# Kernel tuning notes

Measured on AMD Instinct MI355X. Metric: run time of the kernel, lower is better.

## Reference

```python
import jax, jax.numpy as jnp
import numpy as np

D_MODEL = 1024
NUM_HEADS = 16
HEAD_DIM = D_MODEL // NUM_HEADS


def setup_inputs() -> dict:
    key = jax.random.key(0)
    ks = jax.random.split(key, 5)
    x = jax.random.normal(ks[0], (2, 2048, D_MODEL), dtype=jnp.float32)
    # torch nn.Linear init scale ~ U(-1/sqrt(in), 1/sqrt(in)); use small normals
    s = 1.0 / np.sqrt(D_MODEL)
    W_qkv = jax.random.normal(ks[1], (D_MODEL, 3 * D_MODEL), dtype=jnp.float32) * s
    b_qkv = jax.random.normal(ks[2], (3 * D_MODEL,), dtype=jnp.float32) * s
    W_out = jax.random.normal(ks[3], (D_MODEL, D_MODEL), dtype=jnp.float32) * s
    b_out = jax.random.normal(ks[4], (D_MODEL,), dtype=jnp.float32) * s
    return {"x": x, "W_qkv": W_qkv, "b_qkv": b_qkv, "W_out": W_out, "b_out": b_out}


def reference(x, W_qkv, b_qkv, W_out, b_out):
    B, S, _ = x.shape
    qkv = x @ W_qkv + b_qkv                                  # [B,S,3D]
    qkv = qkv.reshape(B, S, NUM_HEADS, 3 * HEAD_DIM).transpose(0, 2, 1, 3)  # [B,H,S,3d]
    q, k, v = jnp.split(qkv, 3, axis=-1)                     # each [B,H,S,d]
    scale = 1.0 / np.sqrt(HEAD_DIM)
    scores = jnp.einsum("bhqd,bhkd->bhqk", q, k) * scale      # [B,H,S,S]
    attn = jax.nn.softmax(scores, axis=-1)
    values = jnp.einsum("bhqk,bhkd->bhqd", attn, v)           # [B,H,S,d]
    values = values.transpose(0, 2, 1, 3).reshape(B, S, D_MODEL)
    return values @ W_out + b_out
```

## Files before the change

### kernel.cpp

```cpp
#include <hip/hip_runtime.h>


#define D_MODEL 1024
#define NHEAD   16
#define HDIM    64
#define SEQ     2048
#define BATCH   2
#define NTOK    (BATCH * SEQ)

typedef float    f32x4 __attribute__((ext_vector_type(4)));
typedef _Float16 f16x8 __attribute__((ext_vector_type(8)));
typedef _Float16 f16x4 __attribute__((ext_vector_type(4)));

#define GLOBAL_LOAD_LDS16(gptr, lptr)                                            \
    __builtin_amdgcn_global_load_lds(                                            \
        (const __attribute__((address_space(1))) unsigned int*)(gptr),           \
        (__attribute__((address_space(3))) unsigned int*)(lptr), 16, 0, 0)

__global__ __launch_bounds__(256) void prep_kernel(
    const float* __restrict__ x, _Float16* __restrict__ xh,
    const float* __restrict__ Wqkv, _Float16* __restrict__ wq_t,
    const float* __restrict__ Wout, _Float16* __restrict__ wo_t)
{
    const int bx = blockIdx.x;
    const int tid = threadIdx.x;
    if (bx < 4096) {
        const int i = (bx * 256 + tid) * 4;
        const float4 v = *(const float4*)&x[i];
        f16x4 hh;
        hh[0] = (_Float16)v.x; hh[1] = (_Float16)v.y;
        hh[2] = (_Float16)v.z; hh[3] = (_Float16)v.w;
        *(f16x4*)&xh[i] = hh;
        return;
    }
    __shared__ float ts[64][65];
    const float* W; _Float16* Wt; int N, n0, k0;
    if (bx < 4096 + 768) {
        const int local = bx - 4096;
        W = Wqkv; Wt = wq_t; N = 3072;
        n0 = (local % 48) * 64; k0 = (local / 48) * 64;
    } else {
        const int local = bx - 4864;
        W = Wout; Wt = wo_t; N = 1024;
        n0 = (local % 16) * 64; k0 = (local / 16) * 64;
    }
    {
        const int r = tid >> 2, c = (tid & 3) << 4;
        const float* src = W + (size_t)(k0 + r) * N + n0 + c;
        #pragma unroll
        for (int u = 0; u < 4; ++u)
            *(float4*)&ts[r][c + u * 4] = *(const float4*)&src[u * 4];
    }
    __syncthreads();
    {
        const int n = tid >> 2, kg = (tid & 3) << 4;
        f16x8 v0, v1;
        #pragma unroll
        for (int j = 0; j < 8; ++j) {
            v0[j] = (_Float16)ts[kg + j][n];
            v1[j] = (_Float16)ts[kg + 8 + j][n];
        }
        _Float16* dst = Wt + (size_t)(n0 + n) * D_MODEL + k0 + kg;
        *(f16x8*)&dst[0] = v0;
        *(f16x8*)&dst[8] = v1;
    }
}

__global__ __launch_bounds__(512) void gemm_qkv_kernel(
    const _Float16* __restrict__ A, const _Float16* __restrict__ Bt,
    const float* __restrict__ bias, _Float16* __restrict__ Cout,
    int M, int N, int K)
{
    __shared__ _Float16 lds[2][4096];
    const int tid = threadIdx.x;
    const int wave = tid >> 6, lane = tid & 63;
    const int quad = lane >> 4, l16 = lane & 15;
    const int m0 = blockIdx.y * 128, n0 = blockIdx.x * 128;
    const int wr = wave >> 1, wc = wave & 1;

    f32x4 acc[2][4] = {};

    const bool isA = wave < 4;
    const _Float16* gsrc = isA ? (A + (size_t)m0 * K) : (Bt + (size_t)n0 * K);
    _Float16* ldst = isA ? &lds[0][0] : &lds[1][0];
    const int sbase = (wave & 3) * 2;

    for (int k0 = 0; k0 < K; k0 += 32) {
        __syncthreads();
        #pragma unroll
        for (int j = 0; j < 2; ++j) {
            const int seg = sbase + j;
            const int chunk = seg >> 1;
            const int row = ((seg & 1) << 6) | lane;
            GLOBAL_LOAD_LDS16(gsrc + (size_t)row * K + k0 + chunk * 8, ldst + seg * 512);
        }
        __syncthreads();

        f16x8 a[2], b[4];
        #pragma unroll
        for (int mt = 0; mt < 2; ++mt)
            a[mt] = *(const f16x8*)&lds[0][quad * 1024 + (wr * 32 + mt * 16 + l16) * 8];
        #pragma unroll
        for (int nt = 0; nt < 4; ++nt)
            b[nt] = *(const f16x8*)&lds[1][quad * 1024 + (wc * 64 + nt * 16 + l16) * 8];
        #pragma unroll
        for (int mt = 0; mt < 2; ++mt)
            #pragma unroll
            for (int nt = 0; nt < 4; ++nt)
                acc[mt][nt] = __builtin_amdgcn_mfma_f32_16x16x32_f16(a[mt], b[nt], acc[mt][nt], 0, 0, 0);
    }

    #pragma unroll
    for (int nt = 0; nt < 4; ++nt) {
        const int col = n0 + wc * 64 + nt * 16 + l16;
        const float bv = bias[col];
        #pragma unroll
        for (int mt = 0; mt < 2; ++mt) {
            #pragma unroll
            for (int r = 0; r < 4; ++r) {
                const int row = m0 + wr * 32 + mt * 16 + quad * 4 + r;
                Cout[(size_t)row * N + col] = (_Float16)(acc[mt][nt][r] + bv);
            }
        }
    }
}

__global__ __launch_bounds__(512) void gemm_out_kernel(
    const _Float16* __restrict__ A, const _Float16* __restrict__ Bt,
    const float* __restrict__ bias, float* __restrict__ Cout)
{
    const int K = D_MODEL, N = D_MODEL;
    __shared__ _Float16 ldsA[4096];
    __shared__ _Float16 ldsB[2048];
    const int tid = threadIdx.x;
    const int wave = tid >> 6, lane = tid & 63;
    const int quad = lane >> 4, l16 = lane & 15;
    const int m0 = blockIdx.y * 128, n0 = blockIdx.x * 64;
    const int wr = wave >> 1, wc = wave & 1;

    f32x4 acc[2][2] = {};

    for (int k0 = 0; k0 < K; k0 += 32) {
        __syncthreads();
        if (wave < 4) {
            #pragma unroll
            for (int j = 0; j < 2; ++j) {
                const int seg = wave * 2 + j;
                const int chunk = seg >> 1;
                const int row = ((seg & 1) << 6) | lane;
                GLOBAL_LOAD_LDS16(A + (size_t)(m0 + row) * K + k0 + chunk * 8, ldsA + seg * 512);
            }
        } else {
            const int seg = wave - 4;
            GLOBAL_LOAD_LDS16(Bt + (size_t)(n0 + lane) * K + k0 + seg * 8, ldsB + seg * 512);
        }
        __syncthreads();

        f16x8 a[2], b[2];
        #pragma unroll
        for (int mt = 0; mt < 2; ++mt)
            a[mt] = *(const f16x8*)&ldsA[quad * 1024 + (wr * 32 + mt * 16 + l16) * 8];
        #pragma unroll
        for (int nt = 0; nt < 2; ++nt)
            b[nt] = *(const f16x8*)&ldsB[quad * 512 + (wc * 32 + nt * 16 + l16) * 8];
        #pragma unroll
        for (int mt = 0; mt < 2; ++mt)
            #pragma unroll
            for (int nt = 0; nt < 2; ++nt)
                acc[mt][nt] = __builtin_amdgcn_mfma_f32_16x16x32_f16(a[mt], b[nt], acc[mt][nt], 0, 0, 0);
    }

    #pragma unroll
    for (int nt = 0; nt < 2; ++nt) {
        const int col = n0 + wc * 32 + nt * 16 + l16;
        const float bv = bias[col];
        #pragma unroll
        for (int mt = 0; mt < 2; ++mt) {
            #pragma unroll
            for (int r = 0; r < 4; ++r) {
                const int row = m0 + wr * 32 + mt * 16 + quad * 4 + r;
                Cout[(size_t)row * N + col] = acc[mt][nt][r] + bv;
            }
        }
    }
}

__global__ __launch_bounds__(256) void swizzle_kv_kernel(
    const _Float16* __restrict__ qkv,
    _Float16* __restrict__ Ksw, _Float16* __restrict__ Vsw)
{
    __shared__ _Float16 ts[64][72];
    const int tid = threadIdx.x;
    const int s0 = blockIdx.x * 64, h = blockIdx.y, b = blockIdx.z;
    const size_t hsz = (size_t)8 * SEQ * 8;
    _Float16* kh = Ksw + (size_t)(b * NHEAD + h) * hsz;
    _Float16* vh = Vsw + (size_t)(b * NHEAD + h) * hsz;

    {
        const int s = s0 + (tid >> 2);
        const int dg = (tid & 3) << 4;
        const _Float16* src = qkv + (size_t)(b * SEQ + s) * (3 * D_MODEL) + h * (3 * HDIM) + HDIM + dg;
        const f16x8 v0 = *(const f16x8*)&src[0];
        const f16x8 v1 = *(const f16x8*)&src[8];
        const int c0 = dg >> 3;
        *(f16x8*)&kh[((size_t)c0 * SEQ + s) * 8]       = v0;
        *(f16x8*)&kh[((size_t)(c0 + 1) * SEQ + s) * 8] = v1;
    }
    {
        const int s = tid >> 2, dg = (tid & 3) << 4;
        const _Float16* src = qkv + (size_t)(b * SEQ + s0 + s) * (3 * D_MODEL) + h * (3 * HDIM) + 2 * HDIM + dg;
        *(f16x8*)&ts[s][dg]     = *(const f16x8*)&src[0];
        *(f16x8*)&ts[s][dg + 8] = *(const f16x8*)&src[8];
    }
    __syncthreads();
    {
        const int d = tid >> 2, sg = (tid & 3) << 4;
        f16x8 v0, v1;
        #pragma unroll
        for (int j = 0; j < 8; ++j) { v0[j] = ts[sg + j][d]; v1[j] = ts[sg + 8 + j][d]; }
        const int cs0 = (s0 + sg) >> 3;
        *(f16x8*)&vh[((size_t)cs0 * HDIM + d) * 8]       = v0;
        *(f16x8*)&vh[((size_t)(cs0 + 1) * HDIM + d) * 8] = v1;
    }
}

__global__ __launch_bounds__(256) void attn_mfma_kernel(
    const _Float16* __restrict__ qkv,
    const _Float16* __restrict__ Ksw, const _Float16* __restrict__ Vsw,
    _Float16* __restrict__ val)
{
    __shared__ _Float16 Ks[8 * 64 * 8];
    __shared__ _Float16 Vts[8 * 64 * 8];
    __shared__ _Float16 Ps[64 * 72];

    const int tid = threadIdx.x;
    const int wave = tid >> 6, lane = tid & 63;
    const int quad = lane >> 4, l16 = lane & 15;
    const int qt = blockIdx.x, h = blockIdx.y, b = blockIdx.z;
    const int q0 = qt * 64;

    const size_t hsz = (size_t)8 * SEQ * 8;
    const _Float16* kh = Ksw + (size_t)(b * NHEAD + h) * hsz;
    const _Float16* vh = Vsw + (size_t)(b * NHEAD + h) * hsz;

    f16x8 qf[2];
    {
        const int row = q0 + wave * 16 + l16;
        const _Float16* src = qkv + (size_t)(b * SEQ + row) * (3 * D_MODEL) + h * (3 * HDIM) + quad * 8;
        const f16x8 t0 = *(const f16x8*)(src);
        const f16x8 t1 = *(const f16x8*)(src + 32);
        #pragma unroll
        for (int j = 0; j < 8; ++j) {
            qf[0][j] = (_Float16)((float)t0[j] * 0.1803368802f);
            qf[1][j] = (_Float16)((float)t1[j] * 0.1803368802f);
        }
    }

    f32x4 acc[4] = {};
    float rs = 0.f;

    for (int kt = 0; kt < SEQ / 64; ++kt) {
        __syncthreads();
        #pragma unroll
        for (int jj = 0; jj < 2; ++jj) {
            const int c = wave * 2 + jj;
            GLOBAL_LOAD_LDS16(kh + ((size_t)c * SEQ + kt * 64 + lane) * 8, Ks + c * 512);
            GLOBAL_LOAD_LDS16(vh + ((size_t)(kt * 8 + c) * HDIM + lane) * 8, Vts + c * 512);
        }
        __syncthreads();

        f32x4 s[4] = {};
        #pragma unroll
        for (int mt = 0; mt < 4; ++mt) {
            const f16x8 kA0 = *(const f16x8*)&Ks[quad * 512 + (mt * 16 + l16) * 8];
            const f16x8 kA1 = *(const f16x8*)&Ks[(4 + quad) * 512 + (mt * 16 + l16) * 8];
            s[mt] = __builtin_amdgcn_mfma_f32_16x16x32_f16(kA0, qf[0], s[mt], 0, 0, 0);
            s[mt] = __builtin_amdgcn_mfma_f32_16x16x32_f16(kA1, qf[1], s[mt], 0, 0, 0);
        }

        #pragma unroll
        for (int mt = 0; mt < 4; ++mt) {
            const float p0 = __builtin_amdgcn_exp2f(s[mt][0]);
            const float p1 = __builtin_amdgcn_exp2f(s[mt][1]);
            const float p2 = __builtin_amdgcn_exp2f(s[mt][2]);
            const float p3 = __builtin_amdgcn_exp2f(s[mt][3]);
            rs += (p0 + p1) + (p2 + p3);
            uint2 w;
            w.x = __builtin_bit_cast(unsigned, __builtin_amdgcn_cvt_pkrtz(p0, p1));
            w.y = __builtin_bit_cast(unsigned, __builtin_amdgcn_cvt_pkrtz(p2, p3));
            *(uint2*)&Ps[(wave * 16 + l16) * 72 + mt * 16 + quad * 4] = w;
        }

        const f16x8 pA0 = *(const f16x8*)&Ps[(wave * 16 + l16) * 72 + quad * 8];
        const f16x8 pA1 = *(const f16x8*)&Ps[(wave * 16 + l16) * 72 + 32 + quad * 8];
        #pragma unroll
        for (int nt = 0; nt < 4; ++nt) {
            const f16x8 v0 = *(const f16x8*)&Vts[quad * 512 + (nt * 16 + l16) * 8];
            const f16x8 v1 = *(const f16x8*)&Vts[(4 + quad) * 512 + (nt * 16 + l16) * 8];
            acc[nt] = __builtin_amdgcn_mfma_f32_16x16x32_f16(pA0, v0, acc[nt], 0, 0, 0);
            acc[nt] = __builtin_amdgcn_mfma_f32_16x16x32_f16(pA1, v1, acc[nt], 0, 0, 0);
        }
    }

    rs += __shfl_xor(rs, 16);
    rs += __shfl_xor(rs, 32);
    const float inv = 1.f / rs;
    float invr[4];
    #pragma unroll
    for (int r = 0; r < 4; ++r)
        invr[r] = __shfl(inv, quad * 4 + r, 16);

    #pragma unroll
    for (int r = 0; r < 4; ++r) {
        const int row = b * SEQ + q0 + wave * 16 + quad * 4 + r;
        #pragma unroll
        for (int nt = 0; nt < 4; ++nt) {
            const int col = h * HDIM + nt * 16 + l16;
            val[(size_t)row * D_MODEL + col] = (_Float16)(acc[nt][r] * invr[r]);
        }
    }
}

extern "C" void kernel_launch(void* const* d_in, const int* in_sizes, int n_in,
                              void* d_out, int out_size, void* d_ws, size_t ws_size,
                              hipStream_t stream)
{
    const float* x     = (const float*)d_in[0];
    const float* W_qkv = (const float*)d_in[1];
    const float* b_qkv = (const float*)d_in[2];
    const float* W_out = (const float*)d_in[3];
    const float* b_out = (const float*)d_in[4];

    char* ws = (char*)d_ws;
    _Float16* Ksw   = (_Float16*)ws;
    _Float16* val_h = (_Float16*)(ws + (8u << 20));
    _Float16* wq_t  = (_Float16*)(ws + (16u << 20));
    _Float16* wo_t  = (_Float16*)(ws + (22u << 20));
    _Float16* qkv_h = (_Float16*)(ws + (24u << 20));
    _Float16* x_h   = (_Float16*)(ws + (48u << 20));
    _Float16* Vsw   = (_Float16*)(ws + (48u << 20));

    prep_kernel<<<5120, 256, 0, stream>>>(x, x_h, W_qkv, wq_t, W_out, wo_t);
    gemm_qkv_kernel<<<dim3(3 * D_MODEL / 128, NTOK / 128), 512, 0, stream>>>(
        x_h, wq_t, b_qkv, qkv_h, NTOK, 3 * D_MODEL, D_MODEL);
    swizzle_kv_kernel<<<dim3(SEQ / 64, NHEAD, BATCH), 256, 0, stream>>>(qkv_h, Ksw, Vsw);
    attn_mfma_kernel<<<dim3(SEQ / 64, NHEAD, BATCH), 256, 0, stream>>>(qkv_h, Ksw, Vsw, val_h);
    gemm_out_kernel<<<dim3(D_MODEL / 64, NTOK / 128), 512, 0, stream>>>(
        val_h, wo_t, b_out, (float*)d_out);
}
```

Measured before the change: 226.2 us.

## Use 32x32 MFMA, 128-row query tiles, and double-buffered K/V in attention

The attention kernel moves from 16x16x32 to 32x32x16 MFMA instructions, with each wave now owning 32 query rows and each block 128. The grid is halved, so each K/V tile loaded into LDS is reused across twice as many queries. K/V loads into LDS are double-buffered, with the next tile prefetched while the current one is computed, leaving one barrier per iteration instead of two. The softmax still has no max subtraction, as before. The trade-off is fewer blocks (512) for occupancy, more accumulator registers, and more LDS per block.

```diff
diff --git a/kernel.cpp b/kernel.cpp
--- a/kernel.cpp
+++ b/kernel.cpp
@@ -8,9 +8,10 @@
 #define BATCH   2
 #define NTOK    (BATCH * SEQ)
 
-typedef float    f32x4 __attribute__((ext_vector_type(4)));
-typedef _Float16 f16x8 __attribute__((ext_vector_type(8)));
-typedef _Float16 f16x4 __attribute__((ext_vector_type(4)));
+typedef float    f32x4  __attribute__((ext_vector_type(4)));
+typedef float    f32x16 __attribute__((ext_vector_type(16)));
+typedef _Float16 f16x8  __attribute__((ext_vector_type(8)));
+typedef _Float16 f16x4  __attribute__((ext_vector_type(4)));
 
 #define GLOBAL_LOAD_LDS16(gptr, lptr)                                            \
     __builtin_amdgcn_global_load_lds(                                            \
@@ -229,95 +230,118 @@
     const _Float16* __restrict__ Ksw, const _Float16* __restrict__ Vsw,
     _Float16* __restrict__ val)
 {
-    __shared__ _Float16 Ks[8 * 64 * 8];
-    __shared__ _Float16 Vts[8 * 64 * 8];
-    __shared__ _Float16 Ps[64 * 72];
+    __shared__ _Float16 Ks[2][4096];
+    __shared__ _Float16 Vts[2][4096];
+    __shared__ _Float16 Ps[128 * 72];
 
     const int tid = threadIdx.x;
     const int wave = tid >> 6, lane = tid & 63;
-    const int quad = lane >> 4, l16 = lane & 15;
+    const int l31 = lane & 31, hi = lane >> 5;
     const int qt = blockIdx.x, h = blockIdx.y, b = blockIdx.z;
-    const int q0 = qt * 64;
+    const int q0 = qt * 128;
 
     const size_t hsz = (size_t)8 * SEQ * 8;
     const _Float16* kh = Ksw + (size_t)(b * NHEAD + h) * hsz;
     const _Float16* vh = Vsw + (size_t)(b * NHEAD + h) * hsz;
 
-    f16x8 qf[2];
-    {
-        const int row = q0 + wave * 16 + l16;
-        const _Float16* src = qkv + (size_t)(b * SEQ + row) * (3 * D_MODEL) + h * (3 * HDIM) + quad * 8;
-        const f16x8 t0 = *(const f16x8*)(src);
-        const f16x8 t1 = *(const f16x8*)(src + 32);
-        #pragma unroll
-        for (int j = 0; j < 8; ++j) {
-            qf[0][j] = (_Float16)((float)t0[j] * 0.1803368802f);
-            qf[1][j] = (_Float16)((float)t1[j] * 0.1803368802f);
-        }
-    }
-
-    f32x4 acc[4] = {};
+    f16x8 qf[4];
+    {
+        const int row = q0 + wave * 32 + l31;
+        const _Float16* src = qkv + (size_t)(b * SEQ + row) * (3 * D_MODEL) + h * (3 * HDIM) + hi * 8;
+        #pragma unroll
+        for (int kk = 0; kk < 4; ++kk) {
+            const f16x8 t = *(const f16x8*)(src + kk * 16);
+            #pragma unroll
+            for (int j = 0; j < 8; ++j)
+                qf[kk][j] = (_Float16)((float)t[j] * 0.1803368802f);
+        }
+    }
+
+    f32x16 acc0 = {};
+    f32x16 acc1 = {};
     float rs = 0.f;
 
+    _Float16* const psrow = &Ps[(wave * 32 + l31) * 72];
+
+    #pragma unroll
+    for (int jj = 0; jj < 2; ++jj) {
+        const int c = wave * 2 + jj;
+        GLOBAL_LOAD_LDS16(kh + ((size_t)c * SEQ + lane) * 8, &Ks[0][c * 512]);
+        GLOBAL_LOAD_LDS16(vh + ((size_t)c * HDIM + lane) * 8, &Vts[0][c * 512]);
+    }
+    __syncthreads();
+
     for (int kt = 0; kt < SEQ / 64; ++kt) {
-        __syncthreads();
-        #pragma unroll
-        for (int jj = 0; jj < 2; ++jj) {
-            const int c = wave * 2 + jj;
-            GLOBAL_LOAD_LDS16(kh + ((size_t)c * SEQ + kt * 64 + lane) * 8, Ks + c * 512);
-            GLOBAL_LOAD_LDS16(vh + ((size_t)(kt * 8 + c) * HDIM + lane) * 8, Vts + c * 512);
-        }
-        __syncthreads();
-
-        f32x4 s[4] = {};
-        #pragma unroll
-        for (int mt = 0; mt < 4; ++mt) {
-            const f16x8 kA0 = *(const f16x8*)&Ks[quad * 512 + (mt * 16 + l16) * 8];
-            const f16x8 kA1 = *(const f16x8*)&Ks[(4 + quad) * 512 + (mt * 16 + l16) * 8];
-            s[mt] = __builtin_amdgcn_mfma_f32_16x16x32_f16(kA0, qf[0], s[mt], 0, 0, 0);
-            s[mt] = __builtin_amdgcn_mfma_f32_16x16x32_f16(kA1, qf[1], s[mt], 0, 0, 0);
-        }
-
-        #pragma unroll
-        for (int mt = 0; mt < 4; ++mt) {
-            const float p0 = __builtin_amdgcn_exp2f(s[mt][0]);
-            const float p1 = __builtin_amdgcn_exp2f(s[mt][1]);
-            const float p2 = __builtin_amdgcn_exp2f(s[mt][2]);
-            const float p3 = __builtin_amdgcn_exp2f(s[mt][3]);
+        const int cur = kt & 1;
+
+        if (kt + 1 < SEQ / 64) {
+            #pragma unroll
+            for (int jj = 0; jj < 2; ++jj) {
+                const int c = wave * 2 + jj;
+                GLOBAL_LOAD_LDS16(kh + ((size_t)c * SEQ + (kt + 1) * 64 + lane) * 8,
+                                  &Ks[cur ^ 1][c * 512]);
+                GLOBAL_LOAD_LDS16(vh + ((size_t)((kt + 1) * 8 + c) * HDIM + lane) * 8,
+                                  &Vts[cur ^ 1][c * 512]);
+            }
+        }
+
+        f32x16 s0 = {};
+        f32x16 s1 = {};
+        #pragma unroll
+        for (int kk = 0; kk < 4; ++kk) {
+            const f16x8 k0 = *(const f16x8*)&Ks[cur][(kk * 2 + hi) * 512 + l31 * 8];
+            const f16x8 k1 = *(const f16x8*)&Ks[cur][(kk * 2 + hi) * 512 + (32 + l31) * 8];
+            s0 = __builtin_amdgcn_mfma_f32_32x32x16_f16(k0, qf[kk], s0, 0, 0, 0);
+            s1 = __builtin_amdgcn_mfma_f32_32x32x16_f16(k1, qf[kk], s1, 0, 0, 0);
+        }
+
+        #pragma unroll
+        for (int rg = 0; rg < 4; ++rg) {
+            const float p0 = __builtin_amdgcn_exp2f(s0[rg * 4 + 0]);
+            const float p1 = __builtin_amdgcn_exp2f(s0[rg * 4 + 1]);
+            const float p2 = __builtin_amdgcn_exp2f(s0[rg * 4 + 2]);
+            const float p3 = __builtin_amdgcn_exp2f(s0[rg * 4 + 3]);
             rs += (p0 + p1) + (p2 + p3);
             uint2 w;
             w.x = __builtin_bit_cast(unsigned, __builtin_amdgcn_cvt_pkrtz(p0, p1));
             w.y = __builtin_bit_cast(unsigned, __builtin_amdgcn_cvt_pkrtz(p2, p3));
-            *(uint2*)&Ps[(wave * 16 + l16) * 72 + mt * 16 + quad * 4] = w;
-        }
-
-        const f16x8 pA0 = *(const f16x8*)&Ps[(wave * 16 + l16) * 72 + quad * 8];
-        const f16x8 pA1 = *(const f16x8*)&Ps[(wave * 16 + l16) * 72 + 32 + quad * 8];
-        #pragma unroll
-        for (int nt = 0; nt < 4; ++nt) {
-            const f16x8 v0 = *(const f16x8*)&Vts[quad * 512 + (nt * 16 + l16) * 8];
-            const f16x8 v1 = *(const f16x8*)&Vts[(4 + quad) * 512 + (nt * 16 + l16) * 8];
-            acc[nt] = __builtin_amdgcn_mfma_f32_16x16x32_f16(pA0, v0, acc[nt], 0, 0, 0);
-            acc[nt] = __builtin_amdgcn_mfma_f32_16x16x32_f16(pA1, v1, acc[nt], 0, 0, 0);
-        }
-    }
-
-    rs += __shfl_xor(rs, 16);
+            *(uint2*)&psrow[rg * 8 + hi * 4] = w;
+        }
+        #pragma unroll
+        for (int rg = 0; rg < 4; ++rg) {
+            const float p0 = __builtin_amdgcn_exp2f(s1[rg * 4 + 0]);
+            const float p1 = __builtin_amdgcn_exp2f(s1[rg * 4 + 1]);
+            const float p2 = __builtin_amdgcn_exp2f(s1[rg * 4 + 2]);
+            const float p3 = __builtin_amdgcn_exp2f(s1[rg * 4 + 3]);
+            rs += (p0 + p1) + (p2 + p3);
+            uint2 w;
+            w.x = __builtin_bit_cast(unsigned, __builtin_amdgcn_cvt_pkrtz(p0, p1));
+            w.y = __builtin_bit_cast(unsigned, __builtin_amdgcn_cvt_pkrtz(p2, p3));
+            *(uint2*)&psrow[32 + rg * 8 + hi * 4] = w;
+        }
+
+        #pragma unroll
+        for (int ks = 0; ks < 4; ++ks) {
+            const f16x8 pa = *(const f16x8*)&psrow[ks * 16 + hi * 8];
+            const f16x8 v0 = *(const f16x8*)&Vts[cur][(ks * 2 + hi) * 512 + l31 * 8];
+            const f16x8 v1 = *(const f16x8*)&Vts[cur][(ks * 2 + hi) * 512 + (32 + l31) * 8];
+            acc0 = __builtin_amdgcn_mfma_f32_32x32x16_f16(pa, v0, acc0, 0, 0, 0);
+            acc1 = __builtin_amdgcn_mfma_f32_32x32x16_f16(pa, v1, acc1, 0, 0, 0);
+        }
+
+        __syncthreads();
+    }
+
     rs += __shfl_xor(rs, 32);
     const float inv = 1.f / rs;
-    float invr[4];
+
     #pragma unroll
-    for (int r = 0; r < 4; ++r)
-        invr[r] = __shfl(inv, quad * 4 + r, 16);
-
-    #pragma unroll
-    for (int r = 0; r < 4; ++r) {
-        const int row = b * SEQ + q0 + wave * 16 + quad * 4 + r;
-        #pragma unroll
-        for (int nt = 0; nt < 4; ++nt) {
-            const int col = h * HDIM + nt * 16 + l16;
-            val[(size_t)row * D_MODEL + col] = (_Float16)(acc[nt][r] * invr[r]);
-        }
+    for (int r = 0; r < 16; ++r) {
+        const int qo = (r & 3) + 8 * (r >> 2) + 4 * hi;
+        const float invr = __shfl(inv, qo);
+        const int row = b * SEQ + q0 + wave * 32 + qo;
+        val[(size_t)row * D_MODEL + h * HDIM + l31]      = (_Float16)(acc0[r] * invr);
+        val[(size_t)row * D_MODEL + h * HDIM + 32 + l31] = (_Float16)(acc1[r] * invr);
     }
 }
 
@@ -344,7 +368,7 @@
     gemm_qkv_kernel<<<dim3(3 * D_MODEL / 128, NTOK / 128), 512, 0, stream>>>(
         x_h, wq_t, b_qkv, qkv_h, NTOK, 3 * D_MODEL, D_MODEL);
     swizzle_kv_kernel<<<dim3(SEQ / 64, NHEAD, BATCH), 256, 0, stream>>>(qkv_h, Ksw, Vsw);
-    attn_mfma_kernel<<<dim3(SEQ / 64, NHEAD, BATCH), 256, 0, stream>>>(qkv_h, Ksw, Vsw, val_h);
+    attn_mfma_kernel<<<dim3(SEQ / 128, NHEAD, BATCH), 256, 0, stream>>>(qkv_h, Ksw, Vsw, val_h);
     gemm_out_kernel<<<dim3(D_MODEL / 64, NTOK / 128), 512, 0, stream>>>(
         val_h, wo_t, b_out, (float*)d_out);
 }
```

After: 226.8 us. About the same (+0.3%).
